# Kernel tuning notes

Measured on AMD Instinct MI355X. Metric: run time of the kernel, lower is better.

Reference implementation:

```python
import jax, jax.numpy as jnp
import numpy as np

NUM_TAGS = 48
START = 46
STOP = 47
B = 1024
S = 512
NEG_INF = -10000.0


def setup_inputs() -> dict:
    key = jax.random.key(0)
    k1, k2, k3, k4 = jax.random.split(key, 4)
    emissions = jax.random.normal(k1, (B, S, NUM_TAGS), dtype=jnp.float32)
    tags = jax.random.randint(k2, (B, S), 0, 46, dtype=jnp.int32)
    lengths = jax.random.randint(k3, (B,), S // 2, S + 1, dtype=jnp.int32)
    mask = (jnp.arange(S, dtype=jnp.int32)[None, :] < lengths[:, None]).astype(jnp.int32)
    # transitions parameter: uniform(-0.1, 0.1), then constraints from reset_parameters
    transitions = jax.random.uniform(k4, (NUM_TAGS, NUM_TAGS), dtype=jnp.float32,
                                     minval=-0.1, maxval=0.1)
    transitions = transitions.at[:, START].set(NEG_INF).at[STOP, :].set(NEG_INF)
    return {"emissions": emissions, "tags": tags, "mask": mask, "transitions": transitions}


def _log_sum_exp(x, axis):
    # matches torch helper: max + log(clamp(sum(exp(x - max)), 1e-10))
    m = jnp.max(x, axis=axis, keepdims=True)
    s = jnp.sum(jnp.exp(x - m), axis=axis, keepdims=True)
    return jnp.squeeze(m + jnp.log(jnp.clip(s, 1e-10)), axis=axis)


def _forward_alg(emissions, transitions, mask):
    b, s, t = emissions.shape
    alpha0 = jnp.full((b, t), NEG_INF, dtype=emissions.dtype).at[:, START].set(0.0)

    def step(alpha, xs):
        emit, m = xs  # emit: (B, T), m: (B,)
        # (B, prev, next)
        nxt = alpha[:, :, None] + transitions[None, :, :] + emit[:, None, :]
        alpha_t = _log_sum_exp(nxt, axis=1)
        alpha = jnp.where(m[:, None] > 0, alpha_t, alpha)
        return alpha, None

    alpha, _ = jax.lax.scan(step, alpha0,
                            (jnp.transpose(emissions, (1, 0, 2)), mask.T))
    terminal = alpha + transitions[STOP][None, :]
    return _log_sum_exp(terminal, axis=1)  # (B,)


def _score_sequence(emissions, transitions, tags, mask):
    b, s, _ = emissions.shape
    start_col = jnp.full((b, 1), START, dtype=tags.dtype)
    tws = jnp.concatenate([start_col, tags], axis=1)  # (B, S+1)
    # transitions[next, prev] per the original _score_sequence
    trans_sc = transitions[tws[:, 1:], tws[:, :-1]]  # (B, S)
    emit_sc = jnp.take_along_axis(emissions, tags[:, :, None].astype(jnp.int32), axis=2)[..., 0]
    score = jnp.sum((trans_sc + emit_sc) * mask.astype(emissions.dtype), axis=1)
    lengths = jnp.sum(mask, axis=1)
    last_tags = jnp.take_along_axis(tags, (lengths - 1)[:, None], axis=1)[:, 0]
    return score + transitions[STOP, last_tags]


def reference(emissions, tags, mask, transitions):
    log_z = _forward_alg(emissions, transitions, mask)
    gold = _score_sequence(emissions, transitions, tags, mask)
    return jnp.mean(log_z - gold)
```

## Files before the change

### kernel.cpp

```cpp
#include <hip/hip_runtime.h>
#include <hip/hip_bf16.h>
#include <stdint.h>
#include <math.h>

#define SLEN 512
#define NT 48
#define TAG_START 46
#define TAG_STOP 47

typedef __attribute__((ext_vector_type(8))) short bf16x8;
typedef __attribute__((ext_vector_type(4))) float f32x4;

typedef const uint32_t __attribute__((address_space(1)))* gptr_t;
typedef uint32_t __attribute__((address_space(3)))* lptr_t;

__device__ __forceinline__ float bcastf(float v, int l) {
  return __int_as_float(__builtin_amdgcn_readlane(__float_as_int(v), l));
}
__device__ __forceinline__ void gload16(const float* g, float* l) {
  __builtin_amdgcn_global_load_lds((gptr_t)(uintptr_t)g, (lptr_t)(uintptr_t)l,
                                   16, 0, 0);
}
__device__ __forceinline__ uint32_t pk2(float a, float b) {
  float2 f;
  f.x = a;
  f.y = b;
  __hip_bfloat162 bb = __float22bfloat162_rn(f);
  uint32_t u;
  __builtin_memcpy(&u, &bb, 4);
  return u;
}

__global__ __launch_bounds__(64) void crf_fwd_kernel(
    const float* __restrict__ em, const int* __restrict__ tags,
    const int* __restrict__ mask, const float* __restrict__ Tr,
    float* __restrict__ ws) {
  const int b = blockIdx.x;
  const int lane = threadIdx.x;
  const int g = lane >> 4;
  const int n = lane & 15;
  __shared__ __align__(16) float lem[2][64 * NT];

  const int* mrow = mask + (size_t)b * SLEN;
  int lc = 0;
  for (int t = lane; t < SLEN; t += 64) lc += mrow[t];
#pragma unroll
  for (int d = 32; d >= 1; d >>= 1) lc += __shfl_xor(lc, d);
  const int len = lc;

  bf16x8 A[3][2];
#pragma unroll
  for (int t = 0; t < 3; ++t) {
#pragma unroll
    for (int c = 0; c < 2; ++c) {
      union { uint32_t u[4]; bf16x8 v; } tmp;
#pragma unroll
      for (int ep = 0; ep < 4; ++ep) {
        float fe[2];
#pragma unroll
        for (int h = 0; h < 2; ++h) {
          const int e = 2 * ep + h;
          const int kl = (e < 4) ? (4 * g + e) : (16 + 4 * g + (e - 4));
          const int ig = 32 * c + kl;
          fe[h] = (ig < NT) ? __expf(Tr[ig * NT + 16 * t + n]) : 0.0f;
        }
        tmp.u[ep] = pk2(fe[0], fe[1]);
      }
      A[t][c] = tmp.v;
    }
  }

  f32x4 v0 = {0.f, 0.f, 0.f, 0.f}, v1 = v0, v2 = v0;
  if (lane == 48) v2.z = 1.0f;
  int cbits = 0;

  const float* embase = em + (size_t)b * SLEN * NT;

  auto dostep = [&](const float* xb) {
    union { uint32_t u[4]; bf16x8 v; } B0, B1;
    B0.u[0] = pk2(v0.x, v0.y);
    B0.u[1] = pk2(v0.z, v0.w);
    B0.u[2] = pk2(v1.x, v1.y);
    B0.u[3] = pk2(v1.z, v1.w);
    B1.u[0] = pk2(v2.x, v2.y);
    B1.u[1] = pk2(v2.z, v2.w);
    B1.u[2] = 0u;
    B1.u[3] = 0u;
    const f32x4 z4 = {0.f, 0.f, 0.f, 0.f};
    f32x4 a0 = __builtin_amdgcn_mfma_f32_16x16x32_bf16(A[0][0], B0.v, z4, 0, 0, 0);
    f32x4 a1 = __builtin_amdgcn_mfma_f32_16x16x32_bf16(A[1][0], B0.v, z4, 0, 0, 0);
    f32x4 a2 = __builtin_amdgcn_mfma_f32_16x16x32_bf16(A[2][0], B0.v, z4, 0, 0, 0);
    a0 = __builtin_amdgcn_mfma_f32_16x16x32_bf16(A[0][1], B1.v, a0, 0, 0, 0);
    a1 = __builtin_amdgcn_mfma_f32_16x16x32_bf16(A[1][1], B1.v, a1, 0, 0, 0);
    a2 = __builtin_amdgcn_mfma_f32_16x16x32_bf16(A[2][1], B1.v, a2, 0, 0, 0);
    const f32x4 x0 = *(const f32x4*)(xb + 4 * g);
    const f32x4 x1 = *(const f32x4*)(xb + 16 + 4 * g);
    const f32x4 x2 = *(const f32x4*)(xb + 32 + 4 * g);
    v0 = a0 * x0;
    v1 = a1 * x1;
    v2 = a2 * x2;
  };

  auto renorm = [&]() {
    f32x4 m4 = __builtin_elementwise_max(__builtin_elementwise_max(v0, v1), v2);
    float m = fmaxf(fmaxf(m4.x, m4.y), fmaxf(m4.z, fmaxf(m4.w, 1e-30f)));
    m = fmaxf(fmaxf(bcastf(m, 0), bcastf(m, 16)),
              fmaxf(bcastf(m, 32), bcastf(m, 48)));
    int ex;
    (void)frexpf(m, &ex);
    const float sc = ldexpf(1.0f, -ex);
    v0 *= sc;
    v1 *= sc;
    v2 *= sc;
    cbits += ex;
  };

  const int nchunks = (len + 63) >> 6;
#pragma unroll
  for (int k = 0; k < 12; ++k)
    gload16(embase + k * 256 + lane * 4, &lem[0][k * 256]);

  for (int c = 0; c < nchunks; ++c) {
    asm volatile("s_waitcnt vmcnt(0)" ::: "memory");
    if (c + 1 < nchunks) {
      const float* src = embase + (size_t)(c + 1) * 64 * NT;
#pragma unroll
      for (int k = 0; k < 12; ++k)
        gload16(src + k * 256 + lane * 4, &lem[(c + 1) & 1][k * 256]);
    }
    float* bufm = lem[c & 1];
    {
      float* row = bufm + lane * NT;
#pragma unroll
      for (int r = 0; r < 12; ++r) {
        f32x4 vx = *(f32x4*)(row + 4 * r);
        vx.x = __expf(vx.x);
        vx.y = __expf(vx.y);
        vx.z = __expf(vx.z);
        vx.w = __expf(vx.w);
        *(f32x4*)(row + 4 * r) = vx;
      }
    }
    const int tend = (len - c * 64 < 64) ? (len - c * 64) : 64;
    int tt = 0;
    for (; tt + 8 <= tend; tt += 8) {
#pragma unroll
      for (int u2 = 0; u2 < 8; ++u2) dostep(bufm + (tt + u2) * NT);
      renorm();
    }
    for (; tt < tend; ++tt) dostep(bufm + tt * NT);
    renorm();
  }

  renorm();
  float zsum = (v0.x + v0.y + v0.z + v0.w) + (v1.x + v1.y + v1.z + v1.w) +
               (v2.x + v2.y + v2.z + v2.w);
#pragma unroll
  for (int d = 32; d >= 1; d >>= 1) zsum += __shfl_xor(zsum, d);
  const float logZ =
      __logf(zsum) + (float)cbits * 0.69314718055994531f + Tr[TAG_STOP * NT];

  const int* trow = tags + (size_t)b * SLEN;
  float gsc = 0.f;
  for (int t = lane; t < len; t += 64) {
    const int tag = trow[t];
    const int prev = (t == 0) ? TAG_START : trow[t - 1];
    gsc += Tr[tag * NT + prev] + embase[(size_t)t * NT + tag];
  }
#pragma unroll
  for (int d = 32; d >= 1; d >>= 1) gsc += __shfl_xor(gsc, d);

  if (lane == 0) {
    const int last = trow[len - 1];
    ws[b] = logZ - (gsc + Tr[TAG_STOP * NT + last]);
  }
}

__global__ void crf_reduce_kernel(const float* __restrict__ ws,
                                  float* __restrict__ out, int n) {
  const int tid = threadIdx.x;
  float v = (tid < n) ? ws[tid] : 0.f;
#pragma unroll
  for (int d = 32; d >= 1; d >>= 1) v += __shfl_xor(v, d);
  __shared__ float part[16];
  if ((tid & 63) == 0) part[tid >> 6] = v;
  __syncthreads();
  if (tid == 0) {
    float s = 0.f;
    for (int i = 0; i < 16; ++i) s += part[i];
    out[0] = s / (float)n;
  }
}

extern "C" void kernel_launch(void* const* d_in, const int* in_sizes, int n_in,
                              void* d_out, int out_size, void* d_ws, size_t ws_size,
                              hipStream_t stream) {
  const float* em = (const float*)d_in[0];
  const int* tags = (const int*)d_in[1];
  const int* mask = (const int*)d_in[2];
  const float* Tr = (const float*)d_in[3];
  const int B = in_sizes[0] / (SLEN * NT);

  float* ws = (float*)d_ws;
  crf_fwd_kernel<<<B, 64, 0, stream>>>(em, tags, mask, Tr, ws);
  crf_reduce_kernel<<<1, 1024, 0, stream>>>(ws, (float*)d_out, B);
}
```

Measured before the change: 97.33 us.

## Software-pipeline LDS emission loads and split MFMA dependency chain in CRF forward

Emission rows for full 64-step chunks are now preloaded from LDS into registers in double-buffered blocks of four steps, so LDS reads overlap the MFMA recurrence. The two chained MFMAs per tile become independent MFMAs whose results are added, which shortens the serial dependency per step at the cost of extra VALU adds. Renormalization uses bit manipulation instead of frexp/ldexp. The exp pass over the LDS chunk uses a lane-contiguous access pattern. Partial chunks renormalize every four steps. Register pressure rises, and launch bounds now request one block per CU.

```diff
diff --git a/kernel.cpp b/kernel.cpp
--- a/kernel.cpp
+++ b/kernel.cpp
@@ -31,7 +31,22 @@
   return u;
 }
 
-__global__ __launch_bounds__(64) void crf_fwd_kernel(
+#define LOADBLK(X, xb)                                   \
+  {                                                      \
+    _Pragma("unroll") for (int u = 0; u < 4; ++u) {      \
+      const float* rp_ = (xb) + u * NT;                  \
+      X[3 * u + 0] = *(const f32x4*)(rp_ + 4 * g);       \
+      X[3 * u + 1] = *(const f32x4*)(rp_ + 16 + 4 * g);  \
+      X[3 * u + 2] = *(const f32x4*)(rp_ + 32 + 4 * g);  \
+    }                                                    \
+  }
+#define STEP4(X)                                         \
+  {                                                      \
+    _Pragma("unroll") for (int u = 0; u < 4; ++u)        \
+        dostep(X[3 * u + 0], X[3 * u + 1], X[3 * u + 2]); \
+  }
+
+__global__ __launch_bounds__(64, 1) void crf_fwd_kernel(
     const float* __restrict__ em, const int* __restrict__ tags,
     const int* __restrict__ mask, const float* __restrict__ Tr,
     float* __restrict__ ws) {
@@ -76,7 +91,7 @@
 
   const float* embase = em + (size_t)b * SLEN * NT;
 
-  auto dostep = [&](const float* xb) {
+  auto dostep = [&](f32x4 x0, f32x4 x1, f32x4 x2) {
     union { uint32_t u[4]; bf16x8 v; } B0, B1;
     B0.u[0] = pk2(v0.x, v0.y);
     B0.u[1] = pk2(v0.z, v0.w);
@@ -87,18 +102,15 @@
     B1.u[2] = 0u;
     B1.u[3] = 0u;
     const f32x4 z4 = {0.f, 0.f, 0.f, 0.f};
-    f32x4 a0 = __builtin_amdgcn_mfma_f32_16x16x32_bf16(A[0][0], B0.v, z4, 0, 0, 0);
-    f32x4 a1 = __builtin_amdgcn_mfma_f32_16x16x32_bf16(A[1][0], B0.v, z4, 0, 0, 0);
-    f32x4 a2 = __builtin_amdgcn_mfma_f32_16x16x32_bf16(A[2][0], B0.v, z4, 0, 0, 0);
-    a0 = __builtin_amdgcn_mfma_f32_16x16x32_bf16(A[0][1], B1.v, a0, 0, 0, 0);
-    a1 = __builtin_amdgcn_mfma_f32_16x16x32_bf16(A[1][1], B1.v, a1, 0, 0, 0);
-    a2 = __builtin_amdgcn_mfma_f32_16x16x32_bf16(A[2][1], B1.v, a2, 0, 0, 0);
-    const f32x4 x0 = *(const f32x4*)(xb + 4 * g);
-    const f32x4 x1 = *(const f32x4*)(xb + 16 + 4 * g);
-    const f32x4 x2 = *(const f32x4*)(xb + 32 + 4 * g);
-    v0 = a0 * x0;
-    v1 = a1 * x1;
-    v2 = a2 * x2;
+    f32x4 p0 = __builtin_amdgcn_mfma_f32_16x16x32_bf16(A[0][0], B0.v, z4, 0, 0, 0);
+    f32x4 p1 = __builtin_amdgcn_mfma_f32_16x16x32_bf16(A[1][0], B0.v, z4, 0, 0, 0);
+    f32x4 p2 = __builtin_amdgcn_mfma_f32_16x16x32_bf16(A[2][0], B0.v, z4, 0, 0, 0);
+    f32x4 q0 = __builtin_amdgcn_mfma_f32_16x16x32_bf16(A[0][1], B1.v, z4, 0, 0, 0);
+    f32x4 q1 = __builtin_amdgcn_mfma_f32_16x16x32_bf16(A[1][1], B1.v, z4, 0, 0, 0);
+    f32x4 q2 = __builtin_amdgcn_mfma_f32_16x16x32_bf16(A[2][1], B1.v, z4, 0, 0, 0);
+    v0 = (p0 + q0) * x0;
+    v1 = (p1 + q1) * x1;
+    v2 = (p2 + q2) * x2;
   };
 
   auto renorm = [&]() {
@@ -106,9 +118,8 @@
     float m = fmaxf(fmaxf(m4.x, m4.y), fmaxf(m4.z, fmaxf(m4.w, 1e-30f)));
     m = fmaxf(fmaxf(bcastf(m, 0), bcastf(m, 16)),
               fmaxf(bcastf(m, 32), bcastf(m, 48)));
-    int ex;
-    (void)frexpf(m, &ex);
-    const float sc = ldexpf(1.0f, -ex);
+    const int ex = ((__float_as_int(m) >> 23) & 255) - 126;
+    const float sc = __int_as_float((127 - ex) << 23);
     v0 *= sc;
     v1 *= sc;
     v2 *= sc;
@@ -129,27 +140,38 @@
         gload16(src + k * 256 + lane * 4, &lem[(c + 1) & 1][k * 256]);
     }
     float* bufm = lem[c & 1];
-    {
-      float* row = bufm + lane * NT;
-#pragma unroll
-      for (int r = 0; r < 12; ++r) {
-        f32x4 vx = *(f32x4*)(row + 4 * r);
-        vx.x = __expf(vx.x);
-        vx.y = __expf(vx.y);
-        vx.z = __expf(vx.z);
-        vx.w = __expf(vx.w);
-        *(f32x4*)(row + 4 * r) = vx;
+#pragma unroll
+    for (int r = 0; r < 12; ++r) {
+      f32x4* p = (f32x4*)(bufm + r * 256 + lane * 4);
+      f32x4 vx = *p;
+      vx.x = __expf(vx.x);
+      vx.y = __expf(vx.y);
+      vx.z = __expf(vx.z);
+      vx.w = __expf(vx.w);
+      *p = vx;
+    }
+    const int tend = (len - c * 64 < 64) ? (len - c * 64) : 64;
+    if (tend == 64) {
+      f32x4 XA[12], XB[12];
+      LOADBLK(XA, bufm);
+      for (int blk = 0; blk < 16; blk += 2) {
+        LOADBLK(XB, bufm + (blk + 1) * 4 * NT);
+        STEP4(XA);
+        if (blk + 2 < 16) LOADBLK(XA, bufm + (blk + 2) * 4 * NT);
+        STEP4(XB);
+        renorm();
       }
-    }
-    const int tend = (len - c * 64 < 64) ? (len - c * 64) : 64;
-    int tt = 0;
-    for (; tt + 8 <= tend; tt += 8) {
-#pragma unroll
-      for (int u2 = 0; u2 < 8; ++u2) dostep(bufm + (tt + u2) * NT);
+    } else {
+      for (int t2 = 0; t2 < tend; ++t2) {
+        const float* rp = bufm + t2 * NT;
+        f32x4 x0 = *(const f32x4*)(rp + 4 * g);
+        f32x4 x1 = *(const f32x4*)(rp + 16 + 4 * g);
+        f32x4 x2 = *(const f32x4*)(rp + 32 + 4 * g);
+        dostep(x0, x1, x2);
+        if ((t2 & 3) == 3) renorm();
+      }
       renorm();
     }
-    for (; tt < tend; ++tt) dostep(bufm + tt * NT);
-    renorm();
   }
 
   renorm();
```

Result: slower. 112.6 us (+15.7%).

## Split CRF forward recursion into concurrent forward and backward halves

Applied to the files above, without the earlier changes.

Replaces the single sequential forward-algorithm chain with a forward pass from the start and a backward pass from the end, each covering half the sequence. The two results are combined with a dot product at the midpoint. Each step now issues two independent MFMA chains, so the serial dependency length is roughly halved and the latency-bound recursion can interleave. The costs are a second set of transposed transition matrices, twice the per-step vector work, an extra step for odd lengths, and a cheaper bit-manipulation renormalisation in place of frexp/ldexp.

```diff
diff --git a/kernel.cpp b/kernel.cpp
--- a/kernel.cpp
+++ b/kernel.cpp
@@ -31,7 +31,7 @@
   return u;
 }
 
-__global__ __launch_bounds__(64) void crf_fwd_kernel(
+__global__ __launch_bounds__(64, 1) void crf_fwd_kernel(
     const float* __restrict__ em, const int* __restrict__ tags,
     const int* __restrict__ mask, const float* __restrict__ Tr,
     float* __restrict__ ws) {
@@ -39,7 +39,8 @@
   const int lane = threadIdx.x;
   const int g = lane >> 4;
   const int n = lane & 15;
-  __shared__ __align__(16) float lem[2][64 * NT];
+  __shared__ __align__(16) float fb[2][32 * NT];
+  __shared__ __align__(16) float bbuf[2][32 * NT];
 
   const int* mrow = mask + (size_t)b * SLEN;
   int lc = 0;
@@ -48,117 +49,211 @@
   for (int d = 32; d >= 1; d >>= 1) lc += __shfl_xor(lc, d);
   const int len = lc;
 
-  bf16x8 A[3][2];
+  bf16x8 Af[3][2], Ab[3][2];
 #pragma unroll
   for (int t = 0; t < 3; ++t) {
 #pragma unroll
     for (int c = 0; c < 2; ++c) {
-      union { uint32_t u[4]; bf16x8 v; } tmp;
+      union { uint32_t u[4]; bf16x8 v; } tf, tb;
 #pragma unroll
       for (int ep = 0; ep < 4; ++ep) {
-        float fe[2];
+        float ff[2], fbk[2];
 #pragma unroll
         for (int h = 0; h < 2; ++h) {
           const int e = 2 * ep + h;
           const int kl = (e < 4) ? (4 * g + e) : (16 + 4 * g + (e - 4));
           const int ig = 32 * c + kl;
-          fe[h] = (ig < NT) ? __expf(Tr[ig * NT + 16 * t + n]) : 0.0f;
+          ff[h] = (ig < NT) ? __expf(Tr[ig * NT + 16 * t + n]) : 0.0f;
+          fbk[h] = (ig < NT) ? __expf(Tr[(16 * t + n) * NT + ig]) : 0.0f;
         }
-        tmp.u[ep] = pk2(fe[0], fe[1]);
+        tf.u[ep] = pk2(ff[0], ff[1]);
+        tb.u[ep] = pk2(fbk[0], fbk[1]);
       }
-      A[t][c] = tmp.v;
+      Af[t][c] = tf.v;
+      Ab[t][c] = tb.v;
     }
   }
 
-  f32x4 v0 = {0.f, 0.f, 0.f, 0.f}, v1 = v0, v2 = v0;
-  if (lane == 48) v2.z = 1.0f;
+  f32x4 vf0 = {0.f, 0.f, 0.f, 0.f}, vf1 = vf0, vf2 = vf0;
+  if (lane == 48) vf2.z = 1.0f;
+  f32x4 vb0 = vf0, vb1 = vf0, vb2 = vf0;
+  if (n == 0) {
+    const f32x4 one4 = {1.f, 1.f, 1.f, 1.f};
+    vb0 = one4;
+    vb1 = one4;
+    vb2 = one4;
+  }
   int cbits = 0;
 
   const float* embase = em + (size_t)b * SLEN * NT;
-
-  auto dostep = [&](const float* xb) {
-    union { uint32_t u[4]; bf16x8 v; } B0, B1;
-    B0.u[0] = pk2(v0.x, v0.y);
-    B0.u[1] = pk2(v0.z, v0.w);
-    B0.u[2] = pk2(v1.x, v1.y);
-    B0.u[3] = pk2(v1.z, v1.w);
-    B1.u[0] = pk2(v2.x, v2.y);
-    B1.u[1] = pk2(v2.z, v2.w);
-    B1.u[2] = 0u;
-    B1.u[3] = 0u;
-    const f32x4 z4 = {0.f, 0.f, 0.f, 0.f};
-    f32x4 a0 = __builtin_amdgcn_mfma_f32_16x16x32_bf16(A[0][0], B0.v, z4, 0, 0, 0);
-    f32x4 a1 = __builtin_amdgcn_mfma_f32_16x16x32_bf16(A[1][0], B0.v, z4, 0, 0, 0);
-    f32x4 a2 = __builtin_amdgcn_mfma_f32_16x16x32_bf16(A[2][0], B0.v, z4, 0, 0, 0);
-    a0 = __builtin_amdgcn_mfma_f32_16x16x32_bf16(A[0][1], B1.v, a0, 0, 0, 0);
-    a1 = __builtin_amdgcn_mfma_f32_16x16x32_bf16(A[1][1], B1.v, a1, 0, 0, 0);
-    a2 = __builtin_amdgcn_mfma_f32_16x16x32_bf16(A[2][1], B1.v, a2, 0, 0, 0);
-    const f32x4 x0 = *(const f32x4*)(xb + 4 * g);
-    const f32x4 x1 = *(const f32x4*)(xb + 16 + 4 * g);
-    const f32x4 x2 = *(const f32x4*)(xb + 32 + 4 * g);
-    v0 = a0 * x0;
-    v1 = a1 * x1;
-    v2 = a2 * x2;
+  const f32x4 z4 = {0.f, 0.f, 0.f, 0.f};
+
+  auto pairstep = [&](const float* xfp, const float* xbp) {
+    const f32x4 xf0 = *(const f32x4*)(xfp + 4 * g);
+    const f32x4 xf1 = *(const f32x4*)(xfp + 16 + 4 * g);
+    const f32x4 xf2 = *(const f32x4*)(xfp + 32 + 4 * g);
+    const f32x4 xb0 = *(const f32x4*)(xbp + 4 * g);
+    const f32x4 xb1 = *(const f32x4*)(xbp + 16 + 4 * g);
+    const f32x4 xb2 = *(const f32x4*)(xbp + 32 + 4 * g);
+    union { uint32_t u[4]; bf16x8 v; } F0, F1;
+    F0.u[0] = pk2(vf0.x, vf0.y);
+    F0.u[1] = pk2(vf0.z, vf0.w);
+    F0.u[2] = pk2(vf1.x, vf1.y);
+    F0.u[3] = pk2(vf1.z, vf1.w);
+    F1.u[0] = pk2(vf2.x, vf2.y);
+    F1.u[1] = pk2(vf2.z, vf2.w);
+    F1.u[2] = 0u;
+    F1.u[3] = 0u;
+    f32x4 af0 = __builtin_amdgcn_mfma_f32_16x16x32_bf16(Af[0][0], F0.v, z4, 0, 0, 0);
+    f32x4 af1 = __builtin_amdgcn_mfma_f32_16x16x32_bf16(Af[1][0], F0.v, z4, 0, 0, 0);
+    f32x4 af2 = __builtin_amdgcn_mfma_f32_16x16x32_bf16(Af[2][0], F0.v, z4, 0, 0, 0);
+    af0 = __builtin_amdgcn_mfma_f32_16x16x32_bf16(Af[0][1], F1.v, af0, 0, 0, 0);
+    af1 = __builtin_amdgcn_mfma_f32_16x16x32_bf16(Af[1][1], F1.v, af1, 0, 0, 0);
+    af2 = __builtin_amdgcn_mfma_f32_16x16x32_bf16(Af[2][1], F1.v, af2, 0, 0, 0);
+    const f32x4 y0 = vb0 * xb0, y1 = vb1 * xb1, y2 = vb2 * xb2;
+    union { uint32_t u[4]; bf16x8 v; } G0, G1;
+    G0.u[0] = pk2(y0.x, y0.y);
+    G0.u[1] = pk2(y0.z, y0.w);
+    G0.u[2] = pk2(y1.x, y1.y);
+    G0.u[3] = pk2(y1.z, y1.w);
+    G1.u[0] = pk2(y2.x, y2.y);
+    G1.u[1] = pk2(y2.z, y2.w);
+    G1.u[2] = 0u;
+    G1.u[3] = 0u;
+    f32x4 ab0 = __builtin_amdgcn_mfma_f32_16x16x32_bf16(Ab[0][0], G0.v, z4, 0, 0, 0);
+    f32x4 ab1 = __builtin_amdgcn_mfma_f32_16x16x32_bf16(Ab[1][0], G0.v, z4, 0, 0, 0);
+    f32x4 ab2 = __builtin_amdgcn_mfma_f32_16x16x32_bf16(Ab[2][0], G0.v, z4, 0, 0, 0);
+    ab0 = __builtin_amdgcn_mfma_f32_16x16x32_bf16(Ab[0][1], G1.v, ab0, 0, 0, 0);
+    ab1 = __builtin_amdgcn_mfma_f32_16x16x32_bf16(Ab[1][1], G1.v, ab1, 0, 0, 0);
+    ab2 = __builtin_amdgcn_mfma_f32_16x16x32_bf16(Ab[2][1], G1.v, ab2, 0, 0, 0);
+    vf0 = af0 * xf0;
+    vf1 = af1 * xf1;
+    vf2 = af2 * xf2;
+    vb0 = ab0;
+    vb1 = ab1;
+    vb2 = ab2;
   };
 
-  auto renorm = [&]() {
-    f32x4 m4 = __builtin_elementwise_max(__builtin_elementwise_max(v0, v1), v2);
-    float m = fmaxf(fmaxf(m4.x, m4.y), fmaxf(m4.z, fmaxf(m4.w, 1e-30f)));
-    m = fmaxf(fmaxf(bcastf(m, 0), bcastf(m, 16)),
-              fmaxf(bcastf(m, 32), bcastf(m, 48)));
-    int ex;
-    (void)frexpf(m, &ex);
-    const float sc = ldexpf(1.0f, -ex);
-    v0 *= sc;
-    v1 *= sc;
-    v2 *= sc;
-    cbits += ex;
+  auto renorm2 = [&]() {
+    f32x4 m4 = __builtin_elementwise_max(__builtin_elementwise_max(vf0, vf1), vf2);
+    float mf = fmaxf(fmaxf(m4.x, m4.y), fmaxf(m4.z, fmaxf(m4.w, 1e-30f)));
+    mf = fmaxf(fmaxf(bcastf(mf, 0), bcastf(mf, 16)),
+               fmaxf(bcastf(mf, 32), bcastf(mf, 48)));
+    const int ef = ((__float_as_int(mf) >> 23) & 255) - 126;
+    const float sf = __int_as_float((127 - ef) << 23);
+    vf0 *= sf;
+    vf1 *= sf;
+    vf2 *= sf;
+    f32x4 n4 = __builtin_elementwise_max(__builtin_elementwise_max(vb0, vb1), vb2);
+    float mb = fmaxf(fmaxf(n4.x, n4.y), fmaxf(n4.z, fmaxf(n4.w, 1e-30f)));
+    mb = fmaxf(fmaxf(bcastf(mb, 0), bcastf(mb, 16)),
+               fmaxf(bcastf(mb, 32), bcastf(mb, 48)));
+    const int eb = ((__float_as_int(mb) >> 23) & 255) - 126;
+    const float sb = __int_as_float((127 - eb) << 23);
+    vb0 *= sb;
+    vb1 *= sb;
+    vb2 *= sb;
+    cbits += ef + eb;
   };
 
-  const int nchunks = (len + 63) >> 6;
-#pragma unroll
-  for (int k = 0; k < 12; ++k)
-    gload16(embase + k * 256 + lane * 4, &lem[0][k * 256]);
-
-  for (int c = 0; c < nchunks; ++c) {
+  const int m = len >> 1;
+  const int nwin = (m + 31) >> 5;
+
+#pragma unroll
+  for (int k = 0; k < 6; ++k) {
+    gload16(embase + k * 256 + lane * 4, &fb[0][k * 256]);
+    gload16(embase + (size_t)(len - 32) * NT + k * 256 + lane * 4,
+            &bbuf[0][k * 256]);
+  }
+
+  for (int c = 0; c < nwin; ++c) {
     asm volatile("s_waitcnt vmcnt(0)" ::: "memory");
-    if (c + 1 < nchunks) {
-      const float* src = embase + (size_t)(c + 1) * 64 * NT;
-#pragma unroll
-      for (int k = 0; k < 12; ++k)
-        gload16(src + k * 256 + lane * 4, &lem[(c + 1) & 1][k * 256]);
-    }
-    float* bufm = lem[c & 1];
-    {
-      float* row = bufm + lane * NT;
-#pragma unroll
-      for (int r = 0; r < 12; ++r) {
-        f32x4 vx = *(f32x4*)(row + 4 * r);
-        vx.x = __expf(vx.x);
-        vx.y = __expf(vx.y);
-        vx.z = __expf(vx.z);
-        vx.w = __expf(vx.w);
-        *(f32x4*)(row + 4 * r) = vx;
+    if (c + 1 < nwin) {
+      const float* fsrc = embase + (size_t)(32 * (c + 1)) * NT;
+      const float* bsrc = embase + (size_t)(len - 32 - 32 * (c + 1)) * NT;
+#pragma unroll
+      for (int k = 0; k < 6; ++k) {
+        gload16(fsrc + k * 256 + lane * 4, &fb[(c + 1) & 1][k * 256]);
+        gload16(bsrc + k * 256 + lane * 4, &bbuf[(c + 1) & 1][k * 256]);
       }
     }
-    const int tend = (len - c * 64 < 64) ? (len - c * 64) : 64;
-    int tt = 0;
-    for (; tt + 8 <= tend; tt += 8) {
-#pragma unroll
-      for (int u2 = 0; u2 < 8; ++u2) dostep(bufm + (tt + u2) * NT);
-      renorm();
+    float* F = fb[c & 1];
+    float* Bw = bbuf[c & 1];
+#pragma unroll
+    for (int r = 0; r < 6; ++r) {
+      f32x4* p = (f32x4*)(F + r * 256 + lane * 4);
+      f32x4 vx = *p;
+      vx.x = __expf(vx.x);
+      vx.y = __expf(vx.y);
+      vx.z = __expf(vx.z);
+      vx.w = __expf(vx.w);
+      *p = vx;
+      f32x4* p2 = (f32x4*)(Bw + r * 256 + lane * 4);
+      f32x4 vy = *p2;
+      vy.x = __expf(vy.x);
+      vy.y = __expf(vy.y);
+      vy.z = __expf(vy.z);
+      vy.w = __expf(vy.w);
+      *p2 = vy;
     }
-    for (; tt < tend; ++tt) dostep(bufm + tt * NT);
-    renorm();
-  }
-
-  renorm();
-  float zsum = (v0.x + v0.y + v0.z + v0.w) + (v1.x + v1.y + v1.z + v1.w) +
-               (v2.x + v2.y + v2.z + v2.w);
-#pragma unroll
-  for (int d = 32; d >= 1; d >>= 1) zsum += __shfl_xor(zsum, d);
+    const int pairs = (m - 32 * c < 32) ? (m - 32 * c) : 32;
+    if (pairs == 32) {
+      for (int uu = 0; uu < 4; ++uu) {
+#pragma unroll
+        for (int u = 0; u < 8; ++u) {
+          const int s = 8 * uu + u;
+          pairstep(F + s * NT, Bw + (31 - s) * NT);
+        }
+        renorm2();
+      }
+    } else {
+      for (int u = 0; u < pairs; ++u) {
+        pairstep(F + u * NT, Bw + (31 - u) * NT);
+        if ((u & 7) == 7) renorm2();
+      }
+      renorm2();
+    }
+  }
+
+  if (len & 1) {
+    const float* rp = embase + (size_t)m * NT;
+    f32x4 xb0 = *(const f32x4*)(rp + 4 * g);
+    f32x4 xb1 = *(const f32x4*)(rp + 16 + 4 * g);
+    f32x4 xb2 = *(const f32x4*)(rp + 32 + 4 * g);
+#define EXP4(v) \
+  v.x = __expf(v.x); v.y = __expf(v.y); v.z = __expf(v.z); v.w = __expf(v.w)
+    EXP4(xb0);
+    EXP4(xb1);
+    EXP4(xb2);
+#undef EXP4
+    const f32x4 y0 = vb0 * xb0, y1 = vb1 * xb1, y2 = vb2 * xb2;
+    union { uint32_t u[4]; bf16x8 v; } G0, G1;
+    G0.u[0] = pk2(y0.x, y0.y);
+    G0.u[1] = pk2(y0.z, y0.w);
+    G0.u[2] = pk2(y1.x, y1.y);
+    G0.u[3] = pk2(y1.z, y1.w);
+    G1.u[0] = pk2(y2.x, y2.y);
+    G1.u[1] = pk2(y2.z, y2.w);
+    G1.u[2] = 0u;
+    G1.u[3] = 0u;
+    f32x4 ab0 = __builtin_amdgcn_mfma_f32_16x16x32_bf16(Ab[0][0], G0.v, z4, 0, 0, 0);
+    f32x4 ab1 = __builtin_amdgcn_mfma_f32_16x16x32_bf16(Ab[1][0], G0.v, z4, 0, 0, 0);
+    f32x4 ab2 = __builtin_amdgcn_mfma_f32_16x16x32_bf16(Ab[2][0], G0.v, z4, 0, 0, 0);
+    ab0 = __builtin_amdgcn_mfma_f32_16x16x32_bf16(Ab[0][1], G1.v, ab0, 0, 0, 0);
+    ab1 = __builtin_amdgcn_mfma_f32_16x16x32_bf16(Ab[1][1], G1.v, ab1, 0, 0, 0);
+    ab2 = __builtin_amdgcn_mfma_f32_16x16x32_bf16(Ab[2][1], G1.v, ab2, 0, 0, 0);
+    vb0 = ab0;
+    vb1 = ab1;
+    vb2 = ab2;
+  }
+
+  renorm2();
+  f32x4 dv = vf0 * vb0 + vf1 * vb1 + vf2 * vb2;
+  float dsum = (dv.x + dv.y) + (dv.z + dv.w);
+#pragma unroll
+  for (int d = 32; d >= 1; d >>= 1) dsum += __shfl_xor(dsum, d);
   const float logZ =
-      __logf(zsum) + (float)cbits * 0.69314718055994531f + Tr[TAG_STOP * NT];
+      __logf(dsum) + (float)cbits * 0.69314718055994531f + Tr[TAG_STOP * NT];
 
   const int* trow = tags + (size_t)b * SLEN;
   float gsc = 0.f;
```

New measurement: 105.2 us. 1.08x slower.

## Split CRF forward recursion into forward and backward halves meeting in the middle

Applied to the files above, without the earlier changes.

Each sequence is now handled by two blocks. One runs the forward alpha recursion over the first half of the valid length, and the other runs a backward beta recursion over the second half using the transposed exp-transition matrix. A new combine kernel takes the dot product of the two vectors and adds the scale exponents to form logZ. This halves the serial dependency chain per block and doubles the grid, in exchange for an extra kernel launch, workspace round-trips, a smaller LDS window per block, and more bf16 rounding paths. Renormalisation also switches from frexpf/ldexpf to direct exponent bit manipulation.

```diff
diff --git a/kernel.cpp b/kernel.cpp
--- a/kernel.cpp
+++ b/kernel.cpp
@@ -7,6 +7,10 @@
 #define NT 48
 #define TAG_START 46
 #define TAG_STOP 47
+
+#define WS_QF 0
+#define WS_WB 65536
+#define WS_OUT 131072
 
 typedef __attribute__((ext_vector_type(8))) short bf16x8;
 typedef __attribute__((ext_vector_type(4))) float f32x4;
@@ -31,15 +35,17 @@
   return u;
 }
 
-__global__ __launch_bounds__(64) void crf_fwd_kernel(
+__global__ __launch_bounds__(64) void crf_split_kernel(
     const float* __restrict__ em, const int* __restrict__ tags,
     const int* __restrict__ mask, const float* __restrict__ Tr,
     float* __restrict__ ws) {
-  const int b = blockIdx.x;
+  const int bid = blockIdx.x;
+  const int b = bid >> 1;
+  const int dir = bid & 1;
   const int lane = threadIdx.x;
   const int g = lane >> 4;
   const int n = lane & 15;
-  __shared__ __align__(16) float lem[2][64 * NT];
+  __shared__ __align__(16) float lem[2][32 * NT];
 
   const int* mrow = mask + (size_t)b * SLEN;
   int lc = 0;
@@ -47,139 +53,256 @@
 #pragma unroll
   for (int d = 32; d >= 1; d >>= 1) lc += __shfl_xor(lc, d);
   const int len = lc;
-
-  bf16x8 A[3][2];
-#pragma unroll
-  for (int t = 0; t < 3; ++t) {
-#pragma unroll
-    for (int c = 0; c < 2; ++c) {
-      union { uint32_t u[4]; bf16x8 v; } tmp;
-#pragma unroll
-      for (int ep = 0; ep < 4; ++ep) {
-        float fe[2];
-#pragma unroll
-        for (int h = 0; h < 2; ++h) {
-          const int e = 2 * ep + h;
-          const int kl = (e < 4) ? (4 * g + e) : (16 + 4 * g + (e - 4));
-          const int ig = 32 * c + kl;
-          fe[h] = (ig < NT) ? __expf(Tr[ig * NT + 16 * t + n]) : 0.0f;
+  const int m = len >> 1;
+
+  const float* embase = em + (size_t)b * SLEN * NT;
+  const f32x4 z4 = {0.f, 0.f, 0.f, 0.f};
+  int cbits = 0;
+
+  if (dir == 0) {
+    bf16x8 A[3][2];
+#pragma unroll
+    for (int t = 0; t < 3; ++t) {
+#pragma unroll
+      for (int c = 0; c < 2; ++c) {
+        union { uint32_t u[4]; bf16x8 v; } tmp;
+#pragma unroll
+        for (int ep = 0; ep < 4; ++ep) {
+          float fe[2];
+#pragma unroll
+          for (int h = 0; h < 2; ++h) {
+            const int e = 2 * ep + h;
+            const int kl = (e < 4) ? (4 * g + e) : (16 + 4 * g + (e - 4));
+            const int ig = 32 * c + kl;
+            fe[h] = (ig < NT) ? __expf(Tr[ig * NT + 16 * t + n]) : 0.0f;
+          }
+          tmp.u[ep] = pk2(fe[0], fe[1]);
         }
-        tmp.u[ep] = pk2(fe[0], fe[1]);
-      }
-      A[t][c] = tmp.v;
-    }
-  }
-
-  f32x4 v0 = {0.f, 0.f, 0.f, 0.f}, v1 = v0, v2 = v0;
-  if (lane == 48) v2.z = 1.0f;
-  int cbits = 0;
-
-  const float* embase = em + (size_t)b * SLEN * NT;
-
-  auto dostep = [&](const float* xb) {
-    union { uint32_t u[4]; bf16x8 v; } B0, B1;
-    B0.u[0] = pk2(v0.x, v0.y);
-    B0.u[1] = pk2(v0.z, v0.w);
-    B0.u[2] = pk2(v1.x, v1.y);
-    B0.u[3] = pk2(v1.z, v1.w);
-    B1.u[0] = pk2(v2.x, v2.y);
-    B1.u[1] = pk2(v2.z, v2.w);
-    B1.u[2] = 0u;
-    B1.u[3] = 0u;
-    const f32x4 z4 = {0.f, 0.f, 0.f, 0.f};
-    f32x4 a0 = __builtin_amdgcn_mfma_f32_16x16x32_bf16(A[0][0], B0.v, z4, 0, 0, 0);
-    f32x4 a1 = __builtin_amdgcn_mfma_f32_16x16x32_bf16(A[1][0], B0.v, z4, 0, 0, 0);
-    f32x4 a2 = __builtin_amdgcn_mfma_f32_16x16x32_bf16(A[2][0], B0.v, z4, 0, 0, 0);
-    a0 = __builtin_amdgcn_mfma_f32_16x16x32_bf16(A[0][1], B1.v, a0, 0, 0, 0);
-    a1 = __builtin_amdgcn_mfma_f32_16x16x32_bf16(A[1][1], B1.v, a1, 0, 0, 0);
-    a2 = __builtin_amdgcn_mfma_f32_16x16x32_bf16(A[2][1], B1.v, a2, 0, 0, 0);
-    const f32x4 x0 = *(const f32x4*)(xb + 4 * g);
-    const f32x4 x1 = *(const f32x4*)(xb + 16 + 4 * g);
-    const f32x4 x2 = *(const f32x4*)(xb + 32 + 4 * g);
-    v0 = a0 * x0;
-    v1 = a1 * x1;
-    v2 = a2 * x2;
-  };
-
-  auto renorm = [&]() {
-    f32x4 m4 = __builtin_elementwise_max(__builtin_elementwise_max(v0, v1), v2);
-    float m = fmaxf(fmaxf(m4.x, m4.y), fmaxf(m4.z, fmaxf(m4.w, 1e-30f)));
-    m = fmaxf(fmaxf(bcastf(m, 0), bcastf(m, 16)),
-              fmaxf(bcastf(m, 32), bcastf(m, 48)));
-    int ex;
-    (void)frexpf(m, &ex);
-    const float sc = ldexpf(1.0f, -ex);
-    v0 *= sc;
-    v1 *= sc;
-    v2 *= sc;
-    cbits += ex;
-  };
-
-  const int nchunks = (len + 63) >> 6;
-#pragma unroll
-  for (int k = 0; k < 12; ++k)
-    gload16(embase + k * 256 + lane * 4, &lem[0][k * 256]);
-
-  for (int c = 0; c < nchunks; ++c) {
-    asm volatile("s_waitcnt vmcnt(0)" ::: "memory");
-    if (c + 1 < nchunks) {
-      const float* src = embase + (size_t)(c + 1) * 64 * NT;
-#pragma unroll
-      for (int k = 0; k < 12; ++k)
-        gload16(src + k * 256 + lane * 4, &lem[(c + 1) & 1][k * 256]);
-    }
-    float* bufm = lem[c & 1];
-    {
-      float* row = bufm + lane * NT;
-#pragma unroll
-      for (int r = 0; r < 12; ++r) {
-        f32x4 vx = *(f32x4*)(row + 4 * r);
+        A[t][c] = tmp.v;
+      }
+    }
+    f32x4 v0 = z4, v1 = z4, v2 = z4;
+    if (lane == 48) v2.z = 1.0f;
+
+    auto dostep = [&](const float* xb) {
+      union { uint32_t u[4]; bf16x8 v; } B0, B1;
+      B0.u[0] = pk2(v0.x, v0.y);
+      B0.u[1] = pk2(v0.z, v0.w);
+      B0.u[2] = pk2(v1.x, v1.y);
+      B0.u[3] = pk2(v1.z, v1.w);
+      B1.u[0] = pk2(v2.x, v2.y);
+      B1.u[1] = pk2(v2.z, v2.w);
+      B1.u[2] = 0u;
+      B1.u[3] = 0u;
+      f32x4 a0 = __builtin_amdgcn_mfma_f32_16x16x32_bf16(A[0][0], B0.v, z4, 0, 0, 0);
+      f32x4 a1 = __builtin_amdgcn_mfma_f32_16x16x32_bf16(A[1][0], B0.v, z4, 0, 0, 0);
+      f32x4 a2 = __builtin_amdgcn_mfma_f32_16x16x32_bf16(A[2][0], B0.v, z4, 0, 0, 0);
+      a0 = __builtin_amdgcn_mfma_f32_16x16x32_bf16(A[0][1], B1.v, a0, 0, 0, 0);
+      a1 = __builtin_amdgcn_mfma_f32_16x16x32_bf16(A[1][1], B1.v, a1, 0, 0, 0);
+      a2 = __builtin_amdgcn_mfma_f32_16x16x32_bf16(A[2][1], B1.v, a2, 0, 0, 0);
+      const f32x4 x0 = *(const f32x4*)(xb + 4 * g);
+      const f32x4 x1 = *(const f32x4*)(xb + 16 + 4 * g);
+      const f32x4 x2 = *(const f32x4*)(xb + 32 + 4 * g);
+      v0 = a0 * x0;
+      v1 = a1 * x1;
+      v2 = a2 * x2;
+    };
+    auto renorm = [&]() {
+      f32x4 m4 = __builtin_elementwise_max(__builtin_elementwise_max(v0, v1), v2);
+      float mx = fmaxf(fmaxf(m4.x, m4.y), fmaxf(m4.z, fmaxf(m4.w, 1e-30f)));
+      mx = fmaxf(fmaxf(bcastf(mx, 0), bcastf(mx, 16)),
+                 fmaxf(bcastf(mx, 32), bcastf(mx, 48)));
+      const int ex = ((__float_as_int(mx) >> 23) & 255) - 126;
+      const float sc = __int_as_float((127 - ex) << 23);
+      v0 *= sc;
+      v1 *= sc;
+      v2 *= sc;
+      cbits += ex;
+    };
+
+    const int nwin = (m + 31) >> 5;
+#pragma unroll
+    for (int k = 0; k < 6; ++k)
+      gload16(embase + k * 256 + lane * 4, &lem[0][k * 256]);
+    for (int c = 0; c < nwin; ++c) {
+      asm volatile("s_waitcnt vmcnt(0)" ::: "memory");
+      if (c + 1 < nwin) {
+        const float* src = embase + (size_t)(32 * (c + 1)) * NT;
+#pragma unroll
+        for (int k = 0; k < 6; ++k)
+          gload16(src + k * 256 + lane * 4, &lem[(c + 1) & 1][k * 256]);
+      }
+      float* buf = lem[c & 1];
+#pragma unroll
+      for (int r = 0; r < 6; ++r) {
+        f32x4* p = (f32x4*)(buf + r * 256 + lane * 4);
+        f32x4 vx = *p;
         vx.x = __expf(vx.x);
         vx.y = __expf(vx.y);
         vx.z = __expf(vx.z);
         vx.w = __expf(vx.w);
-        *(f32x4*)(row + 4 * r) = vx;
-      }
-    }
-    const int tend = (len - c * 64 < 64) ? (len - c * 64) : 64;
-    int tt = 0;
-    for (; tt + 8 <= tend; tt += 8) {
-#pragma unroll
-      for (int u2 = 0; u2 < 8; ++u2) dostep(bufm + (tt + u2) * NT);
-      renorm();
-    }
-    for (; tt < tend; ++tt) dostep(bufm + tt * NT);
-    renorm();
+        *p = vx;
+      }
+      const int steps = (m - 32 * c < 32) ? (m - 32 * c) : 32;
+      for (int s = 0; s < steps; ++s) {
+        dostep(buf + s * NT);
+        if ((s & 7) == 7 || s == steps - 1) renorm();
+      }
+    }
+
+    const int* trow = tags + (size_t)b * SLEN;
+    float gsc = 0.f;
+    for (int t = lane; t < len; t += 64) {
+      const int tag = trow[t];
+      const int prev = (t == 0) ? TAG_START : trow[t - 1];
+      gsc += Tr[tag * NT + prev] + embase[(size_t)t * NT + tag];
+    }
+#pragma unroll
+    for (int d = 32; d >= 1; d >>= 1) gsc += __shfl_xor(gsc, d);
+
+    if (n == 0) {
+      float* dst = ws + WS_QF + (size_t)b * 64;
+      *(f32x4*)(dst + 4 * g) = v0;
+      *(f32x4*)(dst + 16 + 4 * g) = v1;
+      *(f32x4*)(dst + 32 + 4 * g) = v2;
+    }
+    if (lane == 0) {
+      ws[WS_QF + (size_t)b * 64 + 48] = (float)cbits;
+      const int last = trow[len - 1];
+      ws[WS_QF + (size_t)b * 64 + 49] = gsc + Tr[TAG_STOP * NT + last];
+    }
+  } else {
+    bf16x8 A[3][2];
+#pragma unroll
+    for (int t = 0; t < 3; ++t) {
+#pragma unroll
+      for (int c = 0; c < 2; ++c) {
+        union { uint32_t u[4]; bf16x8 v; } tmp;
+#pragma unroll
+        for (int ep = 0; ep < 4; ++ep) {
+          float fe[2];
+#pragma unroll
+          for (int h = 0; h < 2; ++h) {
+            const int e = 2 * ep + h;
+            const int kl = (e < 4) ? (4 * g + e) : (16 + 4 * g + (e - 4));
+            const int ig = 32 * c + kl;
+            fe[h] = (ig < NT) ? __expf(Tr[(16 * t + n) * NT + ig]) : 0.0f;
+          }
+          tmp.u[ep] = pk2(fe[0], fe[1]);
+        }
+        A[t][c] = tmp.v;
+      }
+    }
+    f32x4 v0 = z4, v1 = z4, v2 = z4;
+    if (n == 0) {
+      const f32x4 one4 = {1.f, 1.f, 1.f, 1.f};
+      v0 = one4;
+      v1 = one4;
+      v2 = one4;
+    }
+
+    auto dostep = [&](const float* xb) {
+      const f32x4 x0 = *(const f32x4*)(xb + 4 * g);
+      const f32x4 x1 = *(const f32x4*)(xb + 16 + 4 * g);
+      const f32x4 x2 = *(const f32x4*)(xb + 32 + 4 * g);
+      const f32x4 y0 = v0 * x0, y1 = v1 * x1, y2 = v2 * x2;
+      union { uint32_t u[4]; bf16x8 v; } B0, B1;
+      B0.u[0] = pk2(y0.x, y0.y);
+      B0.u[1] = pk2(y0.z, y0.w);
+      B0.u[2] = pk2(y1.x, y1.y);
+      B0.u[3] = pk2(y1.z, y1.w);
+      B1.u[0] = pk2(y2.x, y2.y);
+      B1.u[1] = pk2(y2.z, y2.w);
+      B1.u[2] = 0u;
+      B1.u[3] = 0u;
+      f32x4 a0 = __builtin_amdgcn_mfma_f32_16x16x32_bf16(A[0][0], B0.v, z4, 0, 0, 0);
+      f32x4 a1 = __builtin_amdgcn_mfma_f32_16x16x32_bf16(A[1][0], B0.v, z4, 0, 0, 0);
+      f32x4 a2 = __builtin_amdgcn_mfma_f32_16x16x32_bf16(A[2][0], B0.v, z4, 0, 0, 0);
+      a0 = __builtin_amdgcn_mfma_f32_16x16x32_bf16(A[0][1], B1.v, a0, 0, 0, 0);
+      a1 = __builtin_amdgcn_mfma_f32_16x16x32_bf16(A[1][1], B1.v, a1, 0, 0, 0);
+      a2 = __builtin_amdgcn_mfma_f32_16x16x32_bf16(A[2][1], B1.v, a2, 0, 0, 0);
+      v0 = a0;
+      v1 = a1;
+      v2 = a2;
+    };
+    auto renorm = [&]() {
+      f32x4 m4 = __builtin_elementwise_max(__builtin_elementwise_max(v0, v1), v2);
+      float mx = fmaxf(fmaxf(m4.x, m4.y), fmaxf(m4.z, fmaxf(m4.w, 1e-30f)));
+      mx = fmaxf(fmaxf(bcastf(mx, 0), bcastf(mx, 16)),
+                 fmaxf(bcastf(mx, 32), bcastf(mx, 48)));
+      const int ex = ((__float_as_int(mx) >> 23) & 255) - 126;
+      const float sc = __int_as_float((127 - ex) << 23);
+      v0 *= sc;
+      v1 *= sc;
+      v2 *= sc;
+      cbits += ex;
+    };
+
+    const int nb = len - m;
+    const int nwin = (nb + 31) >> 5;
+#pragma unroll
+    for (int k = 0; k < 6; ++k)
+      gload16(embase + (size_t)(len - 32) * NT + k * 256 + lane * 4,
+              &lem[0][k * 256]);
+    for (int c = 0; c < nwin; ++c) {
+      asm volatile("s_waitcnt vmcnt(0)" ::: "memory");
+      if (c + 1 < nwin) {
+        const float* src = embase + (size_t)(len - 32 * (c + 2)) * NT;
+#pragma unroll
+        for (int k = 0; k < 6; ++k)
+          gload16(src + k * 256 + lane * 4, &lem[(c + 1) & 1][k * 256]);
+      }
+      float* buf = lem[c & 1];
+#pragma unroll
+      for (int r = 0; r < 6; ++r) {
+        f32x4* p = (f32x4*)(buf + r * 256 + lane * 4);
+        f32x4 vx = *p;
+        vx.x = __expf(vx.x);
+        vx.y = __expf(vx.y);
+        vx.z = __expf(vx.z);
+        vx.w = __expf(vx.w);
+        *p = vx;
+      }
+      const int avail = len - 32 * c - m;
+      const int steps = (avail < 32) ? avail : 32;
+      for (int j = 0; j < steps; ++j) {
+        dostep(buf + (31 - j) * NT);
+        if ((j & 7) == 7 || j == steps - 1) renorm();
+      }
+    }
+
+    if (n == 0) {
+      float* dst = ws + WS_WB + (size_t)b * 64;
+      *(f32x4*)(dst + 4 * g) = v0;
+      *(f32x4*)(dst + 16 + 4 * g) = v1;
+      *(f32x4*)(dst + 32 + 4 * g) = v2;
+    }
+    if (lane == 0) ws[WS_WB + (size_t)b * 64 + 48] = (float)cbits;
   }
-
-  renorm();
-  float zsum = (v0.x + v0.y + v0.z + v0.w) + (v1.x + v1.y + v1.z + v1.w) +
-               (v2.x + v2.y + v2.z + v2.w);
-#pragma unroll
-  for (int d = 32; d >= 1; d >>= 1) zsum += __shfl_xor(zsum, d);
-  const float logZ =
-      __logf(zsum) + (float)cbits * 0.69314718055994531f + Tr[TAG_STOP * NT];
-
-  const int* trow = tags + (size_t)b * SLEN;
-  float gsc = 0.f;
-  for (int t = lane; t < len; t += 64) {
-    const int tag = trow[t];
-    const int prev = (t == 0) ? TAG_START : trow[t - 1];
-    gsc += Tr[tag * NT + prev] + embase[(size_t)t * NT + tag];
+}
+
+__global__ __launch_bounds__(64) void crf_combine_kernel(
+    const float* __restrict__ Tr, float* __restrict__ ws) {
+  const int b = blockIdx.x;
+  const int lane = threadIdx.x;
+  float p = 0.f;
+  if (lane < NT)
+    p = ws[WS_QF + (size_t)b * 64 + lane] * ws[WS_WB + (size_t)b * 64 + lane];
+#pragma unroll
+  for (int d = 32; d >= 1; d >>= 1) p += __shfl_xor(p, d);
+  if (lane == 0) {
+    const float cb =
+        ws[WS_QF + (size_t)b * 64 + 48] + ws[WS_WB + (size_t)b * 64 + 48];
+    const float gold = ws[WS_QF + (size_t)b * 64 + 49];
+    ws[WS_OUT + b] =
+        __logf(p) + cb * 0.69314718055994531f + Tr[TAG_STOP * NT] - gold;
   }
-#pragma unroll
-  for (int d = 32; d >= 1; d >>= 1) gsc += __shfl_xor(gsc, d);
-
-  if (lane == 0) {
-    const int last = trow[len - 1];
-    ws[b] = logZ - (gsc + Tr[TAG_STOP * NT + last]);
-  }
-}
-
-__global__ void crf_reduce_kernel(const float* __restrict__ ws,
+}
+
+__global__ void crf_reduce_kernel(const float* __restrict__ wsrc,
                                   float* __restrict__ out, int n) {
   const int tid = threadIdx.x;
-  float v = (tid < n) ? ws[tid] : 0.f;
+  float v = (tid < n) ? wsrc[tid] : 0.f;
 #pragma unroll
   for (int d = 32; d >= 1; d >>= 1) v += __shfl_xor(v, d);
   __shared__ float part[16];
@@ -202,6 +325,7 @@
   const int B = in_sizes[0] / (SLEN * NT);
 
   float* ws = (float*)d_ws;
-  crf_fwd_kernel<<<B, 64, 0, stream>>>(em, tags, mask, Tr, ws);
-  crf_reduce_kernel<<<1, 1024, 0, stream>>>(ws, (float*)d_out, B);
-}
+  crf_split_kernel<<<2 * B, 64, 0, stream>>>(em, tags, mask, Tr, ws);
+  crf_combine_kernel<<<B, 64, 0, stream>>>(Tr, ws);
+  crf_reduce_kernel<<<1, 1024, 0, stream>>>(ws + WS_OUT, (float*)d_out, B);
+}
```

Measured after the change: 99.98 us. 1.03x slower.
